# Kernel tuning notes

Measured on AMD Instinct MI355X. Metric: run time of the kernel, lower is better.

The kernel has to match this reference:

```python
import jax, jax.numpy as jnp
import numpy as np

# Module config
SIZE = (2, 2)
B, H, W, C = 16, 64, 64, 256


def setup_inputs() -> dict:
    key = jax.random.key(0)
    updates = jax.random.normal(key, (B, H, W, C), dtype=jnp.float32)
    OH, OW = H * SIZE[0], W * SIZE[1]
    # argmax-style mask: flat index into [OH, OW, C] (per-batch), pointing at the
    # top-left element of each pooling window (structure of max_pool_with_argmax)
    h = jnp.arange(H, dtype=jnp.int64)[:, None, None] * SIZE[0]   # [H,1,1]
    w = jnp.arange(W, dtype=jnp.int64)[None, :, None] * SIZE[1]   # [1,W,1]
    c = jnp.arange(C, dtype=jnp.int64)[None, None, :]             # [1,1,C]
    mask = (h * OW + w) * C + c                                   # [H,W,C]
    mask = jnp.broadcast_to(mask, (B, H, W, C))
    return {"updates": updates, "mask": mask}


def reference(updates, mask):
    # Faithful MaxUnpooling2D: scatter pooled values into upsampled output at
    # the positions given by the (per-batch flat) argmax mask; rest are zeros.
    Bv, Hv, Wv, Cv = updates.shape
    OH, OW = Hv * SIZE[0], Wv * SIZE[1]
    flat = OH * OW * Cv
    out = jnp.zeros((Bv, flat), dtype=updates.dtype)
    # tf.scatter_nd sums duplicates into a zero tensor; indices here are unique
    out = out.at[jnp.arange(Bv)[:, None], mask.reshape(Bv, -1)].add(
        updates.reshape(Bv, -1)
    )
    return out.reshape(Bv, OH, OW, Cv)
```

## Files before the change

### kernel.cpp

```cpp
#include <hip/hip_runtime.h>


constexpr int B = 16;
constexpr int H = 64, W = 64, C = 256;
constexpr int IN_PER_BATCH  = H * W * C;
constexpr int OUT_PER_BATCH = (2 * H) * (2 * W) * C;
constexpr long long N_IN = (long long)B * IN_PER_BATCH;

__global__ void unpool_scatter_kernel(const float* __restrict__ updates,
                                      const int* __restrict__ mask,
                                      float* __restrict__ out) {
    long long i = (long long)blockIdx.x * blockDim.x + threadIdx.x;
    if (i >= N_IN) return;
    int b = (int)(i >> 20);
    int m = mask[i];
    out[(long long)b * OUT_PER_BATCH + m] = updates[i];
}

extern "C" void kernel_launch(void* const* d_in, const int* in_sizes, int n_in,
                              void* d_out, int out_size, void* d_ws, size_t ws_size,
                              hipStream_t stream) {
    const float* updates = (const float*)d_in[0];
    const int*   mask    = (const int*)d_in[1];
    float*       out     = (float*)d_out;

    hipMemsetAsync(out, 0, (size_t)out_size * sizeof(float), stream);

    const int block = 256;
    const int grid  = (int)((N_IN + block - 1) / block);
    unpool_scatter_kernel<<<grid, block, 0, stream>>>(updates, mask, out);
}
```

Before: 351.4 us.

## Replace memset plus scatter with a vectorized per-window gather that writes zeros

Drops the separate output memset and the scalar scatter. Each thread now loads four channels of updates and mask as vectors and writes all four positions of its 2x2 output window. Each position gets the update value where the mask matches and zero elsewhere. This removes the extra full-output zeroing pass and the partial-line scattered writes. It assumes each mask index falls inside its own pooling window, which holds for max-pool argmax masks but not for arbitrary indices.

```diff
diff --git a/kernel.cpp b/kernel.cpp
--- a/kernel.cpp
+++ b/kernel.cpp
@@ -3,30 +3,48 @@
 
 constexpr int B = 16;
 constexpr int H = 64, W = 64, C = 256;
-constexpr int IN_PER_BATCH  = H * W * C;
-constexpr int OUT_PER_BATCH = (2 * H) * (2 * W) * C;
-constexpr long long N_IN = (long long)B * IN_PER_BATCH;
+constexpr int OW = 2 * W;
+constexpr int OUT_PER_BATCH = (2 * H) * OW * C;
+constexpr long long N_THREADS = (long long)B * H * W * (C / 4);
 
-__global__ void unpool_scatter_kernel(const float* __restrict__ updates,
-                                      const int* __restrict__ mask,
-                                      float* __restrict__ out) {
-    long long i = (long long)blockIdx.x * blockDim.x + threadIdx.x;
-    if (i >= N_IN) return;
-    int b = (int)(i >> 20);
-    int m = mask[i];
-    out[(long long)b * OUT_PER_BATCH + m] = updates[i];
+__global__ __launch_bounds__(256) void unpool_gather_kernel(
+    const float4* __restrict__ updates4,
+    const int4*   __restrict__ mask4,
+    float*        __restrict__ out) {
+    int t = blockIdx.x * blockDim.x + threadIdx.x;
+    int c4 = t & 63;
+    int w  = (t >> 6) & 63;
+    int h  = (t >> 12) & 63;
+    int b  = t >> 18;
+
+    int4   m = mask4[t];
+    float4 u = updates4[t];
+
+    int base00 = ((h << 1) * OW + (w << 1)) * C + (c4 << 2);
+    float* out_b = out + (long long)b * OUT_PER_BATCH;
+
+    const int ROW = OW * C;
+    #pragma unroll
+    for (int j = 0; j < 4; ++j) {
+        int off = ((j >> 1) ? ROW : 0) + ((j & 1) ? C : 0);
+        int tgt = base00 + off;
+        float4 v;
+        v.x = (m.x == tgt + 0) ? u.x : 0.0f;
+        v.y = (m.y == tgt + 1) ? u.y : 0.0f;
+        v.z = (m.z == tgt + 2) ? u.z : 0.0f;
+        v.w = (m.w == tgt + 3) ? u.w : 0.0f;
+        *(float4*)(out_b + tgt) = v;
+    }
 }
 
 extern "C" void kernel_launch(void* const* d_in, const int* in_sizes, int n_in,
                               void* d_out, int out_size, void* d_ws, size_t ws_size,
                               hipStream_t stream) {
-    const float* updates = (const float*)d_in[0];
-    const int*   mask    = (const int*)d_in[1];
-    float*       out     = (float*)d_out;
-
-    hipMemsetAsync(out, 0, (size_t)out_size * sizeof(float), stream);
+    const float4* updates4 = (const float4*)d_in[0];
+    const int4*   mask4    = (const int4*)d_in[1];
+    float*        out      = (float*)d_out;
 
     const int block = 256;
-    const int grid  = (int)((N_IN + block - 1) / block);
-    unpool_scatter_kernel<<<grid, block, 0, stream>>>(updates, mask, out);
+    const int grid  = (int)(N_THREADS / block);
+    unpool_gather_kernel<<<grid, block, 0, stream>>>(updates4, mask4, out);
 }
```

Result: slower. 358.8 us (+2.1%).
